# Kernel tuning notes

Hardware: AMD Instinct MI355X
Metric: run time of the kernel (lower is better)

## Reference

```python
import jax, jax.numpy as jnp
import numpy as np
from functools import partial

D, H, W = 32, 256, 256   # grid_size (D, H, W)
V = 40000                # number of active voxels
C_IN, C_OUT = 16, 32
K = 3                    # kernel size
P = 32                   # max_points per voxel
EPS = 1e-5               # BatchNorm eps


def setup_inputs() -> dict:
    key = jax.random.key(0)
    k1, k2, k3, k4 = jax.random.split(key, 4)
    voxels = jax.random.normal(k1, (V, C_IN, P), dtype=jnp.float32)
    lin = jax.random.choice(k2, D * H * W, (V,), replace=False)
    d = (lin // (H * W)).astype(jnp.int32)
    h = ((lin // W) % H).astype(jnp.int32)
    w = (lin % W).astype(jnp.int32)
    indices = jnp.stack([w, h, d], axis=1)  # columns are (w, h, d) per original usage
    conv_w = jax.random.normal(k3, (C_OUT, C_IN, K, K, K), dtype=jnp.float32) * 0.05
    conv_b = jax.random.normal(k4, (C_OUT,), dtype=jnp.float32) * 0.05
    gamma = jnp.ones((C_OUT,), dtype=jnp.float32)
    beta = jnp.zeros((C_OUT,), dtype=jnp.float32)
    return {"voxels": voxels, "indices": indices, "conv_w": conv_w,
            "conv_b": conv_b, "gamma": gamma, "beta": beta, "batch_size": 1}


def reference(voxels, indices, conv_w, conv_b, gamma, beta, batch_size):
    # voxel features: mean over points  [V, C]
    feats = voxels.mean(axis=2)
    w_i, h_i, d_i = indices[:, 0], indices[:, 1], indices[:, 2]
    # original: batch_mask = indices[:,0] >= 0, plus per-dim bounds check
    valid = ((w_i >= 0) & (w_i < W) & (h_i >= 0) & (h_i < H) & (d_i >= 0) & (d_i < D))
    d_s = jnp.where(valid, d_i, D)  # route invalid rows out-of-bounds -> dropped
    # fused scatter replacing the python per-voxel loop; [D, H, W, C]
    grid = jnp.zeros((D, H, W, C_IN), dtype=voxels.dtype).at[d_s, h_i, w_i].set(
        feats, mode="drop")
    # same scatter is written into every batch slice in the original
    dense = jnp.broadcast_to(jnp.transpose(grid, (3, 0, 1, 2))[None],
                             (batch_size, C_IN, D, H, W))
    # Conv3d, padding = K//2 (SAME)
    out = jax.lax.conv_general_dilated(
        dense, conv_w, window_strides=(1, 1, 1), padding=[(K // 2, K // 2)] * 3,
        dimension_numbers=("NCDHW", "OIDHW", "NCDHW"))
    out = out + conv_b[None, :, None, None, None]
    # BatchNorm3d (training-mode batch statistics, biased variance)
    mean = out.mean(axis=(0, 2, 3, 4), keepdims=True)
    var = out.var(axis=(0, 2, 3, 4), keepdims=True)
    out = (out - mean) * jax.lax.rsqrt(var + EPS)
    out = out * gamma[None, :, None, None, None] + beta[None, :, None, None, None]
    return jax.nn.relu(out)
```

## Files before the change

kernel.cpp:

```cpp
#include <hip/hip_runtime.h>

#define D_   32
#define H_   256
#define W_   256
#define HW_  (H_ * W_)
#define DHW_ (D_ * H_ * W_)
#define V_   40000
#define CIN  16
#define COUT 32
#define P_   32
#define EPS_ 1e-5f

#define TD 2
#define TH 8
#define TW 32
#define NTX (W_ / TW)
#define NTY (H_ / TH)
#define NTZ (D_ / TD)
#define NT  (NTX * NTY * NTZ)
#define TPOS (TD * TH * TW)
#define OH 16
#define TAP_CAP 768

__global__ void bin_count_kernel(const int* __restrict__ idxs, int* __restrict__ counts) {
    int v = blockIdx.x * 256 + threadIdx.x;
    if (v >= V_) return;
    int w = idxs[3 * v], h = idxs[3 * v + 1], d = idxs[3 * v + 2];
    if ((unsigned)w < W_ && (unsigned)h < H_ && (unsigned)d < D_) {
        int b = (d / TD) * NTY * NTX + (h / TH) * NTX + (w / TW);
        atomicAdd(&counts[b], 1);
    }
}

__global__ void scan_kernel(const int* __restrict__ counts, int* __restrict__ starts,
                            int* __restrict__ cursor, const float* __restrict__ conv_w,
                            float4* __restrict__ wt4) {
    __shared__ int part[256];
    int t = threadIdx.x;
    int base = t * 16;
    int s = 0;
    for (int j = 0; j < 16; ++j) s += counts[base + j];
    part[t] = s;
    __syncthreads();
    for (int off = 1; off < 256; off <<= 1) {
        int val = part[t];
        int add = (t >= off) ? part[t - off] : 0;
        __syncthreads();
        part[t] = val + add;
        __syncthreads();
    }
    int run = (t > 0) ? part[t - 1] : 0;
    for (int j = 0; j < 16; ++j) {
        starts[base + j] = run;
        cursor[base + j] = run;
        run += counts[base + j];
    }
    for (int n = t; n < 2 * 27 * 4 * 16; n += 256) {
        int oo = n & 15;
        int jj = (n >> 4) & 3;
        int m  = n >> 6;
        int k  = m % 27;
        int half = m / 27;
        int o = half * 16 + oo;
        float4 wv;
        wv.x = conv_w[(o * CIN + 4 * jj + 0) * 27 + k];
        wv.y = conv_w[(o * CIN + 4 * jj + 1) * 27 + k];
        wv.z = conv_w[(o * CIN + 4 * jj + 2) * 27 + k];
        wv.w = conv_w[(o * CIN + 4 * jj + 3) * 27 + k];
        wt4[n] = wv;
    }
}

__global__ void bin_fill_kernel(const int* __restrict__ idxs, int* __restrict__ cursor,
                                int* __restrict__ pos_packed, int* __restrict__ perm) {
    int v = blockIdx.x * 256 + threadIdx.x;
    if (v >= V_) return;
    int w = idxs[3 * v], h = idxs[3 * v + 1], d = idxs[3 * v + 2];
    if ((unsigned)w < W_ && (unsigned)h < H_ && (unsigned)d < D_) {
        int b = (d / TD) * NTY * NTX + (h / TH) * NTX + (w / TW);
        int p = atomicAdd(&cursor[b], 1);
        pos_packed[p] = (d << 16) | (h << 8) | w;
        perm[v] = p;
    }
}

__global__ void featpack_kernel(const float* __restrict__ vox, const int* __restrict__ idxs,
                                const int* __restrict__ perm, float4* __restrict__ feats4) {
    int idx = blockIdx.x * 256 + threadIdx.x;
    if (idx >= V_ * 4) return;
    int v = idx >> 2, q = idx & 3;
    int w = idxs[3 * v], h = idxs[3 * v + 1], d = idxs[3 * v + 2];
    if (!((unsigned)w < W_ && (unsigned)h < H_ && (unsigned)d < D_)) return;
    int slot = perm[v];
    const float* base = vox + ((size_t)v * CIN + 4 * q) * P_;
    float m[4];
#pragma unroll
    for (int c = 0; c < 4; ++c) {
        const float4* p = (const float4*)(base + c * P_);
        float s = 0.f;
#pragma unroll
        for (int j = 0; j < P_ / 4; ++j) {
            float4 t = p[j];
            s += t.x + t.y + t.z + t.w;
        }
        m[c] = s * (1.0f / (float)P_);
    }
    feats4[slot * 4 + q] = make_float4(m[0], m[1], m[2], m[3]);
}

__global__ void __launch_bounds__(256, 2) tile_conv_kernel(
    const float4* __restrict__ feats4, const float4* __restrict__ wt4,
    const int* __restrict__ starts, const int* __restrict__ counts,
    const int* __restrict__ pos_packed, float* __restrict__ stats,
    float* __restrict__ out)
{
    __shared__ float  tile[TPOS * 16];
    __shared__ float4 wsm4[27 * 4 * 16];
    __shared__ int    taps[TAP_CAP];
    __shared__ int    seg_off[28];
    __shared__ int    seg_gs[27];
    __shared__ float  wsum[4][16], wsq[4][16];
    __shared__ int    ntap;

    int t = threadIdx.x;
    int tile_id = blockIdx.x;
    int half = blockIdx.y;
    int tx = tile_id % NTX, ty = (tile_id / NTX) % NTY, tz = tile_id / (NTX * NTY);
    int w0 = tx * TW, h0 = ty * TH, d0 = tz * TD;
    int obase = half * OH;

    for (int j = t; j < TPOS * 16 / 4; j += 256) ((float4*)tile)[j] = make_float4(0, 0, 0, 0);
    for (int j = t; j < 27 * 4 * 16; j += 256) wsm4[j] = wt4[half * (27 * 4 * 16) + j];
    if (t < 27) {
        int dz = t / 9 - 1, dy = (t / 3) % 3 - 1, dx = t % 3 - 1;
        int nz = tz + dz, ny = ty + dy, nx = tx + dx;
        int cnt = 0, gs = 0;
        if ((unsigned)nz < NTZ && (unsigned)ny < NTY && (unsigned)nx < NTX) {
            int b = nz * NTY * NTX + ny * NTX + nx;
            gs = starts[b];
            cnt = counts[b];
        }
        seg_gs[t] = gs;
        seg_off[t] = cnt;
    }
    if (t == 0) ntap = 0;
    __syncthreads();
    if (t == 0) {
        int run = 0;
#pragma unroll
        for (int i = 0; i < 27; ++i) {
            int c = seg_off[i];
            seg_off[i] = run;
            run += c;
        }
        seg_off[27] = run;
    }
    __syncthreads();
    int ncand = seg_off[27];

    for (int j = t; j < ncand; j += 256) {
        int b = 0;
        while (seg_off[b + 1] <= j) ++b;
        int src = seg_gs[b] + (j - seg_off[b]);
        int pp = pos_packed[src];
        int vw = pp & 255, vh = (pp >> 8) & 255, vd = pp >> 16;
        int dlo = max(vd - 1, d0), dhi = min(vd + 1, d0 + TD - 1);
        int hlo = max(vh - 1, h0), hhi = min(vh + 1, h0 + TH - 1);
        int wlo = max(vw - 1, w0), whi = min(vw + 1, w0 + TW - 1);
        for (int dq = dlo; dq <= dhi; ++dq)
            for (int hq = hlo; hq <= hhi; ++hq)
                for (int wq = wlo; wq <= whi; ++wq) {
                    int k = ((vd - dq + 1) * 3 + (vh - hq + 1)) * 3 + (vw - wq + 1);
                    int pos = ((dq - d0) * TH + (hq - h0)) * TW + (wq - w0);
                    int slot2 = atomicAdd(&ntap, 1);
                    if (slot2 < TAP_CAP) taps[slot2] = (src << 14) | (k << 9) | pos;
                }
    }
    __syncthreads();
    int nt = min(ntap, TAP_CAP);

    int oo = t & 15;
    int slot = t >> 4;
    for (int j = slot; j < nt; j += 16) {
        unsigned tap = (unsigned)taps[j];
        int pos = tap & 511;
        int k = (tap >> 9) & 31;
        int src = tap >> 14;
        const float4* fp = feats4 + src * 4;
        float4 f0 = fp[0], f1 = fp[1], f2 = fp[2], f3 = fp[3];
        const float4* wp = &wsm4[(k * 4) * 16 + oo];
        float4 q0 = wp[0], q1 = wp[16], q2 = wp[32], q3 = wp[48];
        float acc = q0.x * f0.x + q0.y * f0.y + q0.z * f0.z + q0.w * f0.w
                  + q1.x * f1.x + q1.y * f1.y + q1.z * f1.z + q1.w * f1.w
                  + q2.x * f2.x + q2.y * f2.y + q2.z * f2.z + q2.w * f2.w
                  + q3.x * f3.x + q3.y * f3.y + q3.z * f3.z + q3.w * f3.w;
        atomicAdd(&tile[pos * 16 + (oo ^ (pos & 15))], acc);
    }
    __syncthreads();

    float s1 = 0.f, s2 = 0.f;
    for (int p = slot; p < TPOS; p += 16) {
        float sv = tile[p * 16 + (oo ^ (p & 15))];
        s1 += sv;
        s2 += sv * sv;
    }
    s1 += __shfl_xor(s1, 16); s2 += __shfl_xor(s2, 16);
    s1 += __shfl_xor(s1, 32); s2 += __shfl_xor(s2, 32);
    int wave = t >> 6, lane = t & 63;
    if (lane < 16) { wsum[wave][lane] = s1; wsq[wave][lane] = s2; }

    int wl = t & 31;
    for (int r = t >> 5; r < OH * TD * TH; r += 8) {
        int oo2 = r >> 4;
        int rem = r & 15;
        int pos = rem * TW + wl;
        int dl = rem >> 3, hl = rem & 7;
        out[(size_t)(obase + oo2) * DHW_ + (size_t)(d0 + dl) * HW_ +
            (size_t)(h0 + hl) * W_ + (w0 + wl)] = tile[pos * 16 + (oo2 ^ (pos & 15))];
    }
    __syncthreads();
    if (t < 16) {
        float a = wsum[0][t] + wsum[1][t] + wsum[2][t] + wsum[3][t];
        float b = wsq[0][t] + wsq[1][t] + wsq[2][t] + wsq[3][t];
        atomicAdd(&stats[obase + t], a);
        atomicAdd(&stats[COUT + obase + t], b);
    }
}

__global__ void finalize_kernel(const float* __restrict__ stats,
                                const float* __restrict__ gamma,
                                const float* __restrict__ beta,
                                float* __restrict__ mi) {
    int t = threadIdx.x;
    if (t < COUT) {
        float n = (float)DHW_;
        float m1 = stats[t] / n;
        float m2 = stats[COUT + t] / n;
        float var = fmaxf(m2 - m1 * m1, 0.f);
        float inv = rsqrtf(var + EPS_);
        float A = gamma[t] * inv;
        mi[t] = A;
        mi[COUT + t] = -m1 * A + beta[t];
    }
}

__global__ void norm_kernel(float* __restrict__ out, const float* __restrict__ mi) {
    int idx4 = blockIdx.x * 256 + threadIdx.x;
    int c = idx4 >> 19;
    float A = mi[c], B = mi[COUT + c];
    float4 x = ((const float4*)out)[idx4];
    x.x = fmaxf(x.x * A + B, 0.f);
    x.y = fmaxf(x.y * A + B, 0.f);
    x.z = fmaxf(x.z * A + B, 0.f);
    x.w = fmaxf(x.w * A + B, 0.f);
    ((float4*)out)[idx4] = x;
}

extern "C" void kernel_launch(void* const* d_in, const int* in_sizes, int n_in,
                              void* d_out, int out_size, void* d_ws, size_t ws_size,
                              hipStream_t stream) {
    const float* voxels  = (const float*)d_in[0];
    const int*   indices = (const int*)  d_in[1];
    const float* conv_w  = (const float*)d_in[2];
    const float* gamma   = (const float*)d_in[4];
    const float* beta    = (const float*)d_in[5];
    float* out = (float*)d_out;

    float4* wt4     = (float4*)d_ws;
    float4* feats4  = wt4 + 3456;
    int*    counts  = (int*)(feats4 + (size_t)V_ * 4);
    int*    starts  = counts + NT;
    int*    cursor  = starts + NT;
    int*    pos_pk  = cursor + NT;
    int*    perm    = pos_pk + V_;
    float*  stats   = (float*)(perm + V_);
    float*  mi      = stats + 2 * COUT;

    hipMemsetAsync(counts, 0, NT * sizeof(int), stream);
    hipMemsetAsync(stats, 0, 2 * COUT * sizeof(float), stream);

    bin_count_kernel<<<(V_ + 255) / 256, 256, 0, stream>>>(indices, counts);
    scan_kernel<<<1, 256, 0, stream>>>(counts, starts, cursor, conv_w, wt4);
    bin_fill_kernel<<<(V_ + 255) / 256, 256, 0, stream>>>(indices, cursor, pos_pk, perm);
    featpack_kernel<<<(V_ * 4 + 255) / 256, 256, 0, stream>>>(voxels, indices, perm, feats4);

    dim3 grid(NT, 2);
    tile_conv_kernel<<<grid, 256, 0, stream>>>(feats4, wt4, starts, counts, pos_pk,
                                               stats, out);
    finalize_kernel<<<1, 64, 0, stream>>>(stats, gamma, beta, mi);

    const int n4 = COUT * DHW_ / 4;
    norm_kernel<<<n4 / 256, 256, 0, stream>>>(out, mi);
}
```

Before: 751.1 us.

## Widen tile conv blocks to 512 threads and cut serial setup phases

```diff
diff --git a/kernel.cpp b/kernel.cpp
--- a/kernel.cpp
+++ b/kernel.cpp
@@ -21,6 +21,7 @@
 #define TPOS (TD * TH * TW)
 #define OH 16
 #define TAP_CAP 768
+#define TCT 512
 
 __global__ void bin_count_kernel(const int* __restrict__ idxs, int* __restrict__ counts) {
     int v = blockIdx.x * 256 + threadIdx.x;
@@ -108,7 +109,7 @@
     feats4[slot * 4 + q] = make_float4(m[0], m[1], m[2], m[3]);
 }
 
-__global__ void __launch_bounds__(256, 2) tile_conv_kernel(
+__global__ void __launch_bounds__(TCT, 4) tile_conv_kernel(
     const float4* __restrict__ feats4, const float4* __restrict__ wt4,
     const int* __restrict__ starts, const int* __restrict__ counts,
     const int* __restrict__ pos_packed, float* __restrict__ stats,
@@ -119,7 +120,7 @@
     __shared__ int    taps[TAP_CAP];
     __shared__ int    seg_off[28];
     __shared__ int    seg_gs[27];
-    __shared__ float  wsum[4][16], wsq[4][16];
+    __shared__ float  wsum[8][16], wsq[8][16];
     __shared__ int    ntap;
 
     int t = threadIdx.x;
@@ -129,59 +130,71 @@
     int w0 = tx * TW, h0 = ty * TH, d0 = tz * TD;
     int obase = half * OH;
 
-    for (int j = t; j < TPOS * 16 / 4; j += 256) ((float4*)tile)[j] = make_float4(0, 0, 0, 0);
-    for (int j = t; j < 27 * 4 * 16; j += 256) wsm4[j] = wt4[half * (27 * 4 * 16) + j];
+    for (int j = t; j < TPOS * 16 / 4; j += TCT) ((float4*)tile)[j] = make_float4(0, 0, 0, 0);
+    for (int j = t; j < 27 * 4 * 16; j += TCT) wsm4[j] = wt4[half * (27 * 4 * 16) + j];
+
+    int segc = 0;
     if (t < 27) {
         int dz = t / 9 - 1, dy = (t / 3) % 3 - 1, dx = t % 3 - 1;
         int nz = tz + dz, ny = ty + dy, nx = tx + dx;
-        int cnt = 0, gs = 0;
+        int gs = 0;
         if ((unsigned)nz < NTZ && (unsigned)ny < NTY && (unsigned)nx < NTX) {
             int b = nz * NTY * NTX + ny * NTX + nx;
             gs = starts[b];
-            cnt = counts[b];
+            segc = counts[b];
         }
         seg_gs[t] = gs;
-        seg_off[t] = cnt;
+    }
+    if (t < 64) {
+        int x = segc;
+        int c0 = x;
+#pragma unroll
+        for (int off = 1; off < 32; off <<= 1) {
+            int y = __shfl_up(x, off);
+            if (t >= off) x += y;
+        }
+        if (t < 27) seg_off[t] = x - c0;
+        if (t == 26) seg_off[27] = x;
     }
     if (t == 0) ntap = 0;
     __syncthreads();
-    if (t == 0) {
-        int run = 0;
+    int ncand = seg_off[27];
+
+    for (int j = t; j < ncand; j += TCT) {
+        int lo = 0, hi = 27;
 #pragma unroll
-        for (int i = 0; i < 27; ++i) {
-            int c = seg_off[i];
-            seg_off[i] = run;
-            run += c;
-        }
-        seg_off[27] = run;
-    }
-    __syncthreads();
-    int ncand = seg_off[27];
-
-    for (int j = t; j < ncand; j += 256) {
-        int b = 0;
-        while (seg_off[b + 1] <= j) ++b;
+        for (int it = 0; it < 5; ++it) {
+            int mid = (lo + hi) >> 1;
+            if (seg_off[mid] <= j) lo = mid; else hi = mid;
+        }
+        int b = lo;
         int src = seg_gs[b] + (j - seg_off[b]);
         int pp = pos_packed[src];
         int vw = pp & 255, vh = (pp >> 8) & 255, vd = pp >> 16;
         int dlo = max(vd - 1, d0), dhi = min(vd + 1, d0 + TD - 1);
         int hlo = max(vh - 1, h0), hhi = min(vh + 1, h0 + TH - 1);
         int wlo = max(vw - 1, w0), whi = min(vw + 1, w0 + TW - 1);
-        for (int dq = dlo; dq <= dhi; ++dq)
-            for (int hq = hlo; hq <= hhi; ++hq)
-                for (int wq = wlo; wq <= whi; ++wq) {
-                    int k = ((vd - dq + 1) * 3 + (vh - hq + 1)) * 3 + (vw - wq + 1);
-                    int pos = ((dq - d0) * TH + (hq - h0)) * TW + (wq - w0);
-                    int slot2 = atomicAdd(&ntap, 1);
-                    if (slot2 < TAP_CAP) taps[slot2] = (src << 14) | (k << 9) | pos;
-                }
+        int nd = dhi - dlo + 1, nh = hhi - hlo + 1, nw = whi - wlo + 1;
+        if (nd > 0 && nh > 0 && nw > 0) {
+            int npos = nd * nh * nw;
+            int bslot = atomicAdd(&ntap, npos);
+            int i = 0;
+            for (int dq = dlo; dq <= dhi; ++dq)
+                for (int hq = hlo; hq <= hhi; ++hq)
+                    for (int wq = wlo; wq <= whi; ++wq) {
+                        int k = ((vd - dq + 1) * 3 + (vh - hq + 1)) * 3 + (vw - wq + 1);
+                        int pos = ((dq - d0) * TH + (hq - h0)) * TW + (wq - w0);
+                        int s2 = bslot + i; ++i;
+                        if (s2 < TAP_CAP) taps[s2] = (src << 14) | (k << 9) | pos;
+                    }
+        }
     }
     __syncthreads();
     int nt = min(ntap, TAP_CAP);
 
     int oo = t & 15;
     int slot = t >> 4;
-    for (int j = slot; j < nt; j += 16) {
+    for (int j = slot; j < nt; j += 32) {
         unsigned tap = (unsigned)taps[j];
         int pos = tap & 511;
         int k = (tap >> 9) & 31;
@@ -199,7 +212,7 @@
     __syncthreads();
 
     float s1 = 0.f, s2 = 0.f;
-    for (int p = slot; p < TPOS; p += 16) {
+    for (int p = slot; p < TPOS; p += 32) {
         float sv = tile[p * 16 + (oo ^ (p & 15))];
         s1 += sv;
         s2 += sv * sv;
@@ -210,7 +223,7 @@
     if (lane < 16) { wsum[wave][lane] = s1; wsq[wave][lane] = s2; }
 
     int wl = t & 31;
-    for (int r = t >> 5; r < OH * TD * TH; r += 8) {
+    for (int r = t >> 5; r < OH * TD * TH; r += 16) {
         int oo2 = r >> 4;
         int rem = r & 15;
         int pos = rem * TW + wl;
@@ -220,8 +233,10 @@
     }
     __syncthreads();
     if (t < 16) {
-        float a = wsum[0][t] + wsum[1][t] + wsum[2][t] + wsum[3][t];
-        float b = wsq[0][t] + wsq[1][t] + wsq[2][t] + wsq[3][t];
+        float a = wsum[0][t] + wsum[1][t] + wsum[2][t] + wsum[3][t]
+                + wsum[4][t] + wsum[5][t] + wsum[6][t] + wsum[7][t];
+        float b = wsq[0][t] + wsq[1][t] + wsq[2][t] + wsq[3][t]
+                + wsq[4][t] + wsq[5][t] + wsq[6][t] + wsq[7][t];
         atomicAdd(&stats[obase + t], a);
         atomicAdd(&stats[COUT + obase + t], b);
     }
@@ -285,7 +300,7 @@
     featpack_kernel<<<(V_ * 4 + 255) / 256, 256, 0, stream>>>(voxels, indices, perm, feats4);
 
     dim3 grid(NT, 2);
-    tile_conv_kernel<<<grid, 256, 0, stream>>>(feats4, wt4, starts, counts, pos_pk,
+    tile_conv_kernel<<<grid, TCT, 0, stream>>>(feats4, wt4, starts, counts, pos_pk,
                                                stats, out);
     finalize_kernel<<<1, 64, 0, stream>>>(stats, gamma, beta, mi);
 
```

Result: faster. 708.2 us (-5.7%).

## Precompute per-tile tap lists globally and split output channels into quarters

Applied to the files above, without the earlier changes.

```diff
diff --git a/kernel.cpp b/kernel.cpp
--- a/kernel.cpp
+++ b/kernel.cpp
@@ -19,16 +19,23 @@
 #define NTZ (D_ / TD)
 #define NT  (NTX * NTY * NTZ)
 #define TPOS (TD * TH * TW)
-#define OH 16
-#define TAP_CAP 768
-
-__global__ void bin_count_kernel(const int* __restrict__ idxs, int* __restrict__ counts) {
-    int v = blockIdx.x * 256 + threadIdx.x;
-    if (v >= V_) return;
+#define OH 8
+#define NQ (COUT / OH)
+#define TROW 9
+#define TCT 512
+
+__global__ void tap_count_kernel(const int* __restrict__ idxs, int* __restrict__ tapcnt) {
+    int idx = blockIdx.x * 256 + threadIdx.x;
+    if (idx >= V_ * 27) return;
+    int v = idx / 27, kk = idx - v * 27;
     int w = idxs[3 * v], h = idxs[3 * v + 1], d = idxs[3 * v + 2];
-    if ((unsigned)w < W_ && (unsigned)h < H_ && (unsigned)d < D_) {
-        int b = (d / TD) * NTY * NTX + (h / TH) * NTX + (w / TW);
-        atomicAdd(&counts[b], 1);
+    if (!((unsigned)w < W_ && (unsigned)h < H_ && (unsigned)d < D_)) return;
+    int dq = d + kk / 9 - 1;
+    int hq = h + (kk / 3) % 3 - 1;
+    int wq = w + kk % 3 - 1;
+    if ((unsigned)dq < D_ && (unsigned)hq < H_ && (unsigned)wq < W_) {
+        int tile = (dq / TD) * NTY * NTX + (hq / TH) * NTX + (wq / TW);
+        atomicAdd(&tapcnt[tile], 1);
     }
 }
 
@@ -55,13 +62,13 @@
         cursor[base + j] = run;
         run += counts[base + j];
     }
-    for (int n = t; n < 2 * 27 * 4 * 16; n += 256) {
-        int oo = n & 15;
-        int jj = (n >> 4) & 3;
-        int m  = n >> 6;
+    for (int n = t; n < NQ * 27 * 4 * OH; n += 256) {
+        int oo = n & 7;
+        int jj = (n >> 3) & 3;
+        int m  = n >> 5;
         int k  = m % 27;
-        int half = m / 27;
-        int o = half * 16 + oo;
+        int quarter = m / 27;
+        int o = quarter * OH + oo;
         float4 wv;
         wv.x = conv_w[(o * CIN + 4 * jj + 0) * 27 + k];
         wv.y = conv_w[(o * CIN + 4 * jj + 1) * 27 + k];
@@ -71,27 +78,29 @@
     }
 }
 
-__global__ void bin_fill_kernel(const int* __restrict__ idxs, int* __restrict__ cursor,
-                                int* __restrict__ pos_packed, int* __restrict__ perm) {
-    int v = blockIdx.x * 256 + threadIdx.x;
-    if (v >= V_) return;
+__global__ void tap_fill_kernel(const int* __restrict__ idxs, int* __restrict__ cursor,
+                                int* __restrict__ tapbuf) {
+    int idx = blockIdx.x * 256 + threadIdx.x;
+    if (idx >= V_ * 27) return;
+    int v = idx / 27, kk = idx - v * 27;
     int w = idxs[3 * v], h = idxs[3 * v + 1], d = idxs[3 * v + 2];
-    if ((unsigned)w < W_ && (unsigned)h < H_ && (unsigned)d < D_) {
-        int b = (d / TD) * NTY * NTX + (h / TH) * NTX + (w / TW);
-        int p = atomicAdd(&cursor[b], 1);
-        pos_packed[p] = (d << 16) | (h << 8) | w;
-        perm[v] = p;
-    }
-}
-
-__global__ void featpack_kernel(const float* __restrict__ vox, const int* __restrict__ idxs,
-                                const int* __restrict__ perm, float4* __restrict__ feats4) {
+    if (!((unsigned)w < W_ && (unsigned)h < H_ && (unsigned)d < D_)) return;
+    int dq = d + kk / 9 - 1;
+    int hq = h + (kk / 3) % 3 - 1;
+    int wq = w + kk % 3 - 1;
+    if ((unsigned)dq < D_ && (unsigned)hq < H_ && (unsigned)wq < W_) {
+        int tile = (dq / TD) * NTY * NTX + (hq / TH) * NTX + (wq / TW);
+        int pos = ((dq & (TD - 1)) * TH + (hq & (TH - 1))) * TW + (wq & (TW - 1));
+        int k = 26 - kk;
+        int p = atomicAdd(&cursor[tile], 1);
+        tapbuf[p] = (v << 14) | (k << 9) | pos;
+    }
+}
+
+__global__ void featpack_kernel(const float* __restrict__ vox, float4* __restrict__ feats4) {
     int idx = blockIdx.x * 256 + threadIdx.x;
     if (idx >= V_ * 4) return;
     int v = idx >> 2, q = idx & 3;
-    int w = idxs[3 * v], h = idxs[3 * v + 1], d = idxs[3 * v + 2];
-    if (!((unsigned)w < W_ && (unsigned)h < H_ && (unsigned)d < D_)) return;
-    int slot = perm[v];
     const float* base = vox + ((size_t)v * CIN + 4 * q) * P_;
     float m[4];
 #pragma unroll
@@ -105,123 +114,79 @@
         }
         m[c] = s * (1.0f / (float)P_);
     }
-    feats4[slot * 4 + q] = make_float4(m[0], m[1], m[2], m[3]);
-}
-
-__global__ void __launch_bounds__(256, 2) tile_conv_kernel(
+    feats4[v * 4 + q] = make_float4(m[0], m[1], m[2], m[3]);
+}
+
+__global__ void __launch_bounds__(TCT, 8) tile_conv_kernel(
     const float4* __restrict__ feats4, const float4* __restrict__ wt4,
-    const int* __restrict__ starts, const int* __restrict__ counts,
-    const int* __restrict__ pos_packed, float* __restrict__ stats,
+    const int* __restrict__ tapstart, const int* __restrict__ tapcnt,
+    const int* __restrict__ tapbuf, float* __restrict__ stats,
     float* __restrict__ out)
 {
-    __shared__ float  tile[TPOS * 16];
-    __shared__ float4 wsm4[27 * 4 * 16];
-    __shared__ int    taps[TAP_CAP];
-    __shared__ int    seg_off[28];
-    __shared__ int    seg_gs[27];
-    __shared__ float  wsum[4][16], wsq[4][16];
-    __shared__ int    ntap;
+    __shared__ float  tile[TPOS * TROW];
+    __shared__ float4 wsm4[27 * 4 * OH];
+    __shared__ float  wsum[8][OH], wsq[8][OH];
 
     int t = threadIdx.x;
     int tile_id = blockIdx.x;
-    int half = blockIdx.y;
+    int quarter = blockIdx.y;
     int tx = tile_id % NTX, ty = (tile_id / NTX) % NTY, tz = tile_id / (NTX * NTY);
     int w0 = tx * TW, h0 = ty * TH, d0 = tz * TD;
-    int obase = half * OH;
-
-    for (int j = t; j < TPOS * 16 / 4; j += 256) ((float4*)tile)[j] = make_float4(0, 0, 0, 0);
-    for (int j = t; j < 27 * 4 * 16; j += 256) wsm4[j] = wt4[half * (27 * 4 * 16) + j];
-    if (t < 27) {
-        int dz = t / 9 - 1, dy = (t / 3) % 3 - 1, dx = t % 3 - 1;
-        int nz = tz + dz, ny = ty + dy, nx = tx + dx;
-        int cnt = 0, gs = 0;
-        if ((unsigned)nz < NTZ && (unsigned)ny < NTY && (unsigned)nx < NTX) {
-            int b = nz * NTY * NTX + ny * NTX + nx;
-            gs = starts[b];
-            cnt = counts[b];
-        }
-        seg_gs[t] = gs;
-        seg_off[t] = cnt;
-    }
-    if (t == 0) ntap = 0;
-    __syncthreads();
-    if (t == 0) {
-        int run = 0;
-#pragma unroll
-        for (int i = 0; i < 27; ++i) {
-            int c = seg_off[i];
-            seg_off[i] = run;
-            run += c;
-        }
-        seg_off[27] = run;
-    }
-    __syncthreads();
-    int ncand = seg_off[27];
-
-    for (int j = t; j < ncand; j += 256) {
-        int b = 0;
-        while (seg_off[b + 1] <= j) ++b;
-        int src = seg_gs[b] + (j - seg_off[b]);
-        int pp = pos_packed[src];
-        int vw = pp & 255, vh = (pp >> 8) & 255, vd = pp >> 16;
-        int dlo = max(vd - 1, d0), dhi = min(vd + 1, d0 + TD - 1);
-        int hlo = max(vh - 1, h0), hhi = min(vh + 1, h0 + TH - 1);
-        int wlo = max(vw - 1, w0), whi = min(vw + 1, w0 + TW - 1);
-        for (int dq = dlo; dq <= dhi; ++dq)
-            for (int hq = hlo; hq <= hhi; ++hq)
-                for (int wq = wlo; wq <= whi; ++wq) {
-                    int k = ((vd - dq + 1) * 3 + (vh - hq + 1)) * 3 + (vw - wq + 1);
-                    int pos = ((dq - d0) * TH + (hq - h0)) * TW + (wq - w0);
-                    int slot2 = atomicAdd(&ntap, 1);
-                    if (slot2 < TAP_CAP) taps[slot2] = (src << 14) | (k << 9) | pos;
-                }
-    }
-    __syncthreads();
-    int nt = min(ntap, TAP_CAP);
-
-    int oo = t & 15;
-    int slot = t >> 4;
-    for (int j = slot; j < nt; j += 16) {
-        unsigned tap = (unsigned)taps[j];
+    int obase = quarter * OH;
+
+    for (int j = t; j < TPOS * TROW / 4; j += TCT)
+        ((float4*)tile)[j] = make_float4(0, 0, 0, 0);
+    for (int j = t; j < 27 * 4 * OH; j += TCT)
+        wsm4[j] = wt4[quarter * (27 * 4 * OH) + j];
+    int gs = tapstart[tile_id];
+    int nt = tapcnt[tile_id];
+    __syncthreads();
+
+    int oo = t & 7;
+    int slot = t >> 3;
+    for (int j = slot; j < nt; j += 64) {
+        unsigned tap = (unsigned)tapbuf[gs + j];
         int pos = tap & 511;
         int k = (tap >> 9) & 31;
         int src = tap >> 14;
         const float4* fp = feats4 + src * 4;
         float4 f0 = fp[0], f1 = fp[1], f2 = fp[2], f3 = fp[3];
-        const float4* wp = &wsm4[(k * 4) * 16 + oo];
-        float4 q0 = wp[0], q1 = wp[16], q2 = wp[32], q3 = wp[48];
+        const float4* wp = &wsm4[(k * 4) * OH + oo];
+        float4 q0 = wp[0], q1 = wp[8], q2 = wp[16], q3 = wp[24];
         float acc = q0.x * f0.x + q0.y * f0.y + q0.z * f0.z + q0.w * f0.w
                   + q1.x * f1.x + q1.y * f1.y + q1.z * f1.z + q1.w * f1.w
                   + q2.x * f2.x + q2.y * f2.y + q2.z * f2.z + q2.w * f2.w
                   + q3.x * f3.x + q3.y * f3.y + q3.z * f3.z + q3.w * f3.w;
-        atomicAdd(&tile[pos * 16 + (oo ^ (pos & 15))], acc);
+        atomicAdd(&tile[pos * TROW + oo], acc);
     }
     __syncthreads();
 
     float s1 = 0.f, s2 = 0.f;
-    for (int p = slot; p < TPOS; p += 16) {
-        float sv = tile[p * 16 + (oo ^ (p & 15))];
+    for (int p = slot; p < TPOS; p += 64) {
+        float sv = tile[p * TROW + oo];
         s1 += sv;
         s2 += sv * sv;
     }
+    s1 += __shfl_xor(s1, 8);  s2 += __shfl_xor(s2, 8);
     s1 += __shfl_xor(s1, 16); s2 += __shfl_xor(s2, 16);
     s1 += __shfl_xor(s1, 32); s2 += __shfl_xor(s2, 32);
     int wave = t >> 6, lane = t & 63;
-    if (lane < 16) { wsum[wave][lane] = s1; wsq[wave][lane] = s2; }
+    if (lane < OH) { wsum[wave][lane] = s1; wsq[wave][lane] = s2; }
 
     int wl = t & 31;
-    for (int r = t >> 5; r < OH * TD * TH; r += 8) {
+    for (int r = t >> 5; r < OH * TD * TH; r += 16) {
         int oo2 = r >> 4;
         int rem = r & 15;
         int pos = rem * TW + wl;
         int dl = rem >> 3, hl = rem & 7;
         out[(size_t)(obase + oo2) * DHW_ + (size_t)(d0 + dl) * HW_ +
-            (size_t)(h0 + hl) * W_ + (w0 + wl)] = tile[pos * 16 + (oo2 ^ (pos & 15))];
-    }
-    __syncthreads();
-    if (t < 16) {
-        float a = wsum[0][t] + wsum[1][t] + wsum[2][t] + wsum[3][t];
-        float b = wsq[0][t] + wsq[1][t] + wsq[2][t] + wsq[3][t];
+            (size_t)(h0 + hl) * W_ + (w0 + wl)] = tile[pos * TROW + oo2];
+    }
+    __syncthreads();
+    if (t < OH) {
+        float a = 0.f, b = 0.f;
+#pragma unroll
+        for (int wv = 0; wv < 8; ++wv) { a += wsum[wv][t]; b += wsq[wv][t]; }
         atomicAdd(&stats[obase + t], a);
         atomicAdd(&stats[COUT + obase + t], b);
     }
@@ -266,26 +231,26 @@
     const float* beta    = (const float*)d_in[5];
     float* out = (float*)d_out;
 
-    float4* wt4     = (float4*)d_ws;
-    float4* feats4  = wt4 + 3456;
-    int*    counts  = (int*)(feats4 + (size_t)V_ * 4);
-    int*    starts  = counts + NT;
-    int*    cursor  = starts + NT;
-    int*    pos_pk  = cursor + NT;
-    int*    perm    = pos_pk + V_;
-    float*  stats   = (float*)(perm + V_);
-    float*  mi      = stats + 2 * COUT;
-
-    hipMemsetAsync(counts, 0, NT * sizeof(int), stream);
+    float4* wt4      = (float4*)d_ws;
+    float4* feats4   = wt4 + 3456;
+    int*    tapcnt   = (int*)(feats4 + (size_t)V_ * 4);
+    int*    tapstart = tapcnt + NT;
+    int*    tapcur   = tapstart + NT;
+    int*    tapbuf   = tapcur + NT;
+    float*  stats    = (float*)(tapbuf + (size_t)V_ * 27);
+    float*  mi       = stats + 2 * COUT;
+
+    hipMemsetAsync(tapcnt, 0, NT * sizeof(int), stream);
     hipMemsetAsync(stats, 0, 2 * COUT * sizeof(float), stream);
 
-    bin_count_kernel<<<(V_ + 255) / 256, 256, 0, stream>>>(indices, counts);
-    scan_kernel<<<1, 256, 0, stream>>>(counts, starts, cursor, conv_w, wt4);
-    bin_fill_kernel<<<(V_ + 255) / 256, 256, 0, stream>>>(indices, cursor, pos_pk, perm);
-    featpack_kernel<<<(V_ * 4 + 255) / 256, 256, 0, stream>>>(voxels, indices, perm, feats4);
-
-    dim3 grid(NT, 2);
-    tile_conv_kernel<<<grid, 256, 0, stream>>>(feats4, wt4, starts, counts, pos_pk,
+    const int ntap_items = V_ * 27;
+    tap_count_kernel<<<(ntap_items + 255) / 256, 256, 0, stream>>>(indices, tapcnt);
+    scan_kernel<<<1, 256, 0, stream>>>(tapcnt, tapstart, tapcur, conv_w, wt4);
+    tap_fill_kernel<<<(ntap_items + 255) / 256, 256, 0, stream>>>(indices, tapcur, tapbuf);
+    featpack_kernel<<<(V_ * 4 + 255) / 256, 256, 0, stream>>>(voxels, feats4);
+
+    dim3 grid(NT, NQ);
+    tile_conv_kernel<<<grid, TCT, 0, stream>>>(feats4, wt4, tapstart, tapcnt, tapbuf,
                                                stats, out);
     finalize_kernel<<<1, 64, 0, stream>>>(stats, gamma, beta, mi);
 
```

After: 873.5 us. 16.3% more time.
